# Optimization experiments

Hardware: AMD Instinct MI355X
Metric: run time of the kernel (lower is better)

## Reference

```python
import jax, jax.numpy as jnp
import numpy as np

NUM_HEADS = 16
D_MODEL = 1024
D_K = D_MODEL // NUM_HEADS


def setup_inputs() -> dict:
    key = jax.random.key(0)
    ks = jax.random.split(key, 11)
    B, S = 2, 2048
    s = 1.0 / np.sqrt(D_MODEL)
    return {
        "Q": jax.random.normal(ks[0], (B, S, D_MODEL), jnp.float32),
        "K": jax.random.normal(ks[1], (B, S, D_MODEL), jnp.float32),
        "V": jax.random.normal(ks[2], (B, S, D_MODEL), jnp.float32),
        "Wq": jax.random.normal(ks[3], (D_MODEL, D_MODEL), jnp.float32) * s,
        "bq": jnp.zeros((D_MODEL,), jnp.float32),
        "Wk": jax.random.normal(ks[4], (D_MODEL, D_MODEL), jnp.float32) * s,
        "bk": jnp.zeros((D_MODEL,), jnp.float32),
        "Wv": jax.random.normal(ks[5], (D_MODEL, D_MODEL), jnp.float32) * s,
        "bv": jnp.zeros((D_MODEL,), jnp.float32),
        "Wo": jax.random.normal(ks[6], (D_MODEL, D_MODEL), jnp.float32) * s,
        "bo": jnp.zeros((D_MODEL,), jnp.float32),
    }


def _split_heads(x):
    B, S, _ = x.shape
    return x.reshape(B, S, NUM_HEADS, D_K).transpose(0, 2, 1, 3)  # (B,H,S,Dk)


def reference(Q, K, V, Wq, bq, Wk, bk, Wv, bv, Wo, bo):
    q = _split_heads(Q @ Wq + bq)
    k = _split_heads(K @ Wk + bk)
    v = _split_heads(V @ Wv + bv)
    scores = jnp.einsum("bhqd,bhkd->bhqk", q, k) / jnp.sqrt(jnp.asarray(D_K, q.dtype))
    attn = jax.nn.softmax(scores, axis=-1)
    out = jnp.einsum("bhqk,bhkd->bhqd", attn, v)  # (B,H,S,Dk)
    B, H, S, Dk = out.shape
    combined = out.transpose(0, 2, 1, 3).reshape(B, S, H * Dk)
    return combined @ Wo + bo
```

## Files before the change

### kernel.cpp

```cpp
#include <hip/hip_runtime.h>
#include <stdint.h>

#define DM   1024
#define NH   16
#define DKH  64
#define SEQ  2048
#define NB   2

typedef __attribute__((ext_vector_type(8))) short  frag8;
typedef __attribute__((ext_vector_type(4))) short  frag4;
typedef __attribute__((ext_vector_type(4))) short  short4v;
typedef __attribute__((ext_vector_type(8))) short  short8v;
typedef __attribute__((ext_vector_type(4))) float  f32x4;

__device__ __forceinline__ unsigned short f2bf(float x){
  unsigned u = __float_as_uint(x);
  u += 0x7fffu + ((u >> 16) & 1u);
  return (unsigned short)(u >> 16);
}

__device__ __forceinline__ float dev_exp2(float x){
  return __builtin_amdgcn_exp2f(x);
}

#define GLOAD16(GP, LP) __builtin_amdgcn_global_load_lds( \
    (__attribute__((address_space(1))) void*)(GP), \
    (__attribute__((address_space(3))) void*)(LP), 16, 0, 0)

#define LDSFENCE() do{ asm volatile("" ::: "memory"); \
                       __builtin_amdgcn_sched_barrier(0); }while(0)



__global__ __launch_bounds__(256) void cast_qkv(const float* __restrict__ Q,
                                                const float* __restrict__ K,
                                                const float* __restrict__ V,
                                                short* __restrict__ dst){
  const int z = blockIdx.z;
  const float* src = (z == 0) ? Q : (z == 1 ? K : V);
  const int i = (blockIdx.x * 256 + threadIdx.x) * 4;
  float4 f = *(const float4*)(src + i);
  short4v s;
  s.x = (short)f2bf(f.x); s.y = (short)f2bf(f.y);
  s.z = (short)f2bf(f.z); s.w = (short)f2bf(f.w);
  *(short4v*)(dst + (long)z * (SEQ*NB*DM) + i) = s;
}

__global__ __launch_bounds__(256) void wtrans(const float* __restrict__ Wq,
                                              const float* __restrict__ Wk,
                                              const float* __restrict__ Wv,
                                              const float* __restrict__ Wo,
                                              short* __restrict__ wt){
  const int z = blockIdx.z;
  const float* W = (z == 0) ? Wq : (z == 1 ? Wk : (z == 2 ? Wv : Wo));
  short* out = wt + (long)z * (DM*DM);
  __shared__ float t[32][33];
  const int n0 = blockIdx.x * 32, k0 = blockIdx.y * 32;
  const int c = threadIdx.x & 31, r0 = threadIdx.x >> 5;
#pragma unroll
  for (int i = 0; i < 4; ++i){
    int r = r0 + i * 8;
    t[r][c] = W[(k0 + r) * DM + n0 + c];
  }
  __syncthreads();
#pragma unroll
  for (int i = 0; i < 4; ++i){
    int r = r0 + i * 8;
    out[(n0 + r) * DM + k0 + c] = (short)f2bf(t[c][r]);
  }
}

__device__ __forceinline__ void store_out(short* p, float v){ *p = (short)f2bf(v); }
__device__ __forceinline__ void store_out(float* p, float v){ *p = v; }

template<typename OT>
__global__ __launch_bounds__(512) void gemm_bt(const short* __restrict__ Abase, long Astride,
                                               const short* __restrict__ Btbase, long Btstride,
                                               const float* __restrict__ bias0,
                                               const float* __restrict__ bias1,
                                               const float* __restrict__ bias2,
                                               OT* __restrict__ Cbase, long Cstride,
                                               float qscale){
  const int z = blockIdx.z;
  const short* A  = Abase + (long)z * Astride;
  const short* Bt = Btbase + (long)z * Btstride;
  OT* C = Cbase + (long)z * Cstride;
  const float* bias = (z == 0) ? bias0 : (z == 1 ? bias1 : bias2);
  const float scale = (z == 0) ? qscale : 1.0f;
  const int KD = DM, ND = DM;

  __shared__ __align__(16) short As[2][128 * 64];
  __shared__ __align__(16) short Bs[2][128 * 64];

  const int tid = threadIdx.x;
  const int w = tid >> 6, lane = tid & 63, l15 = lane & 15, quad = lane >> 4;
  const int wy = w >> 1, wx = w & 1;
  const int bm = blockIdx.x * 128, bn = blockIdx.y * 128;
  const int lrow = lane >> 3;
  const int lcolsw = (((lane & 7) ^ lrow) & 7) * 8;

  f32x4 acc[2][4] = {};

#define GSTAGE(KT, BSEL) do{                                                    \
  _Pragma("unroll")                                                             \
  for (int i_ = 0; i_ < 2; ++i_){                                               \
    int j_ = w * 2 + i_;                                                        \
    GLOAD16(A  + (bm + j_ * 8 + lrow) * KD + (KT) * 64 + lcolsw,                \
            &As[BSEL][j_ * 512]);                                               \
    GLOAD16(Bt + (bn + j_ * 8 + lrow) * KD + (KT) * 64 + lcolsw,                \
            &Bs[BSEL][j_ * 512]);                                               \
  } }while(0)

#define GCOMPUTE(BS) do{                                                        \
  _Pragma("unroll") for (int ks = 0; ks < 2; ++ks){                             \
    frag8 af[2], bf_[4];                                                        \
    _Pragma("unroll") for (int mt = 0; mt < 2; ++mt)                            \
      af[mt] = *(const frag8*)&As[BS][(wy * 32 + mt * 16 + l15) * 64 +          \
                                      (((ks * 4 + quad) ^ (l15 & 7)) * 8)];     \
    _Pragma("unroll") for (int nt = 0; nt < 4; ++nt)                            \
      bf_[nt] = *(const frag8*)&Bs[BS][(wx * 64 + nt * 16 + l15) * 64 +         \
                                       (((ks * 4 + quad) ^ (l15 & 7)) * 8)];    \
    _Pragma("unroll") for (int mt = 0; mt < 2; ++mt)                            \
      _Pragma("unroll") for (int nt = 0; nt < 4; ++nt)                          \
        acc[mt][nt] = __builtin_amdgcn_mfma_f32_16x16x32_bf16(                  \
            af[mt], bf_[nt], acc[mt][nt], 0, 0, 0);                             \
  } }while(0)

  GSTAGE(0, 0);
  for (int t = 0; t < KD / 64 - 1; ++t){
    GSTAGE(t + 1, (t + 1) & 1);
    asm volatile("s_waitcnt vmcnt(4)" ::: "memory");
    __builtin_amdgcn_s_barrier();
    LDSFENCE();
    GCOMPUTE(t & 1);
    asm volatile("s_waitcnt lgkmcnt(0)" ::: "memory");
    __builtin_amdgcn_sched_barrier(0);
    __builtin_amdgcn_s_barrier();
  }
  asm volatile("s_waitcnt vmcnt(0)" ::: "memory");
  __builtin_amdgcn_s_barrier();
  LDSFENCE();
  GCOMPUTE(1);

#undef GSTAGE
#undef GCOMPUTE

#pragma unroll
  for (int mt = 0; mt < 2; ++mt){
#pragma unroll
    for (int r = 0; r < 4; ++r){
      int m = bm + wy * 32 + mt * 16 + quad * 4 + r;
#pragma unroll
      for (int nt = 0; nt < 4; ++nt){
        int n = bn + wx * 64 + nt * 16 + l15;
        float v = (acc[mt][nt][r] + bias[n]) * scale;
        store_out(&C[(long)m * ND + n], v);
      }
    }
  }
}

template<typename OT>
__global__ __launch_bounds__(512) void gemm64_bt(const short* __restrict__ A,
                                                 const short* __restrict__ Bt,
                                                 const float* __restrict__ bias,
                                                 OT* __restrict__ C,
                                                 float scale){
  const int KD = DM, ND = DM;
  __shared__ __align__(16) short As[2][64 * 64];
  __shared__ __align__(16) short Bs[2][128 * 64];
  const int tid = threadIdx.x;
  const int w = tid >> 6, lane = tid & 63, l15 = lane & 15, quad = lane >> 4;
  const int wy = w >> 1, wx = w & 1;
  const int bm = blockIdx.x * 64, bn = blockIdx.y * 128;
  const int lrow = lane >> 3;
  const int lcolsw = (((lane & 7) ^ lrow) & 7) * 8;
  f32x4 acc[4] = {};

#define GSTAGE64(KT, BSEL) do{                                                  \
  {                                                                             \
    int j_ = w;                                                                 \
    GLOAD16(A + (bm + j_ * 8 + lrow) * KD + (KT) * 64 + lcolsw,                 \
            &As[BSEL][j_ * 512]);                                               \
  }                                                                             \
  _Pragma("unroll")                                                             \
  for (int i_ = 0; i_ < 2; ++i_){                                               \
    int j_ = w * 2 + i_;                                                        \
    GLOAD16(Bt + (bn + j_ * 8 + lrow) * KD + (KT) * 64 + lcolsw,                \
            &Bs[BSEL][j_ * 512]);                                               \
  } }while(0)

#define GCOMPUTE64(BS) do{                                                      \
  _Pragma("unroll") for (int ks = 0; ks < 2; ++ks){                             \
    frag8 af, bf_[4];                                                           \
    af = *(const frag8*)&As[BS][(wy * 16 + l15) * 64 +                          \
                                (((ks * 4 + quad) ^ (l15 & 7)) * 8)];           \
    _Pragma("unroll") for (int nt = 0; nt < 4; ++nt)                            \
      bf_[nt] = *(const frag8*)&Bs[BS][(wx * 64 + nt * 16 + l15) * 64 +         \
                                       (((ks * 4 + quad) ^ (l15 & 7)) * 8)];    \
    _Pragma("unroll") for (int nt = 0; nt < 4; ++nt)                            \
      acc[nt] = __builtin_amdgcn_mfma_f32_16x16x32_bf16(                        \
          af, bf_[nt], acc[nt], 0, 0, 0);                                       \
  } }while(0)

  GSTAGE64(0, 0);
  for (int t = 0; t < KD / 64 - 1; ++t){
    GSTAGE64(t + 1, (t + 1) & 1);
    asm volatile("s_waitcnt vmcnt(3)" ::: "memory");
    __builtin_amdgcn_s_barrier();
    LDSFENCE();
    GCOMPUTE64(t & 1);
    asm volatile("s_waitcnt lgkmcnt(0)" ::: "memory");
    __builtin_amdgcn_sched_barrier(0);
    __builtin_amdgcn_s_barrier();
  }
  asm volatile("s_waitcnt vmcnt(0)" ::: "memory");
  __builtin_amdgcn_s_barrier();
  LDSFENCE();
  GCOMPUTE64(1);

#undef GSTAGE64
#undef GCOMPUTE64

#pragma unroll
  for (int r = 0; r < 4; ++r){
    int m = bm + wy * 16 + quad * 4 + r;
#pragma unroll
    for (int nt = 0; nt < 4; ++nt){
      int n = bn + wx * 64 + nt * 16 + l15;
      store_out(&C[(long)m * ND + n], (acc[nt][r] + bias[n]) * scale);
    }
  }
}

__global__ __launch_bounds__(256) void vtrans(const short* __restrict__ v,
                                              short* __restrict__ vt){
  const int bh = blockIdx.y;
  const int b = bh >> 4, h = bh & 15;
  const int s0 = blockIdx.x * 64;
  __shared__ short tT[64][66];
  const short* vb = v + ((long)(b * SEQ + s0)) * DM + h * DKH;
  for (int j = threadIdx.x; j < 512; j += 256){
    int row = j >> 3, off = (j & 7) * 8;
    short8v d = *(const short8v*)(vb + row * DM + off);
#pragma unroll
    for (int e = 0; e < 8; ++e) tT[off + e][row] = d[e];
  }
  __syncthreads();
  short* out = vt + (long)bh * (DKH * SEQ) + s0;
  for (int j = threadIdx.x; j < 512; j += 256){
    int dr = j >> 3, soff = (j & 7) * 8;
    short8v o;
#pragma unroll
    for (int e = 0; e < 8; ++e) o[e] = tT[dr][soff + e];
    *(short8v*)(out + dr * SEQ + soff) = o;
  }
}

__global__ __launch_bounds__(512) void flash(const short* __restrict__ q,
                                             const short* __restrict__ k,
                                             const short* __restrict__ vt,
                                             short* __restrict__ comb){
  const int bh = blockIdx.y;
  const int b = bh >> 4, h = bh & 15;
  const int q0 = blockIdx.x * 128;
  const int tid = threadIdx.x;
  const int w = tid >> 6, lane = tid & 63, l15 = lane & 15, quad = lane >> 4;

  __shared__ __align__(16) short Ks[3][64 * 64];
  __shared__ __align__(16) short Vs[3][64 * 64];

  frag8 aq[2];
  const short* qb = q + ((long)(b * SEQ + q0 + w * 16)) * DM + h * DKH;
#pragma unroll
  for (int ks = 0; ks < 2; ++ks)
    aq[ks] = *(const frag8*)(qb + l15 * DM + ks * 32 + quad * 8);

  frag8 ones8;
#pragma unroll
  for (int e = 0; e < 8; ++e) ones8[e] = (short)0x3F80;

  f32x4 O[4] = {};
  f32x4 Lacc = {0.f, 0.f, 0.f, 0.f};

  const short* kb  = k + ((long)b * SEQ) * DM + h * DKH;
  const short* vtb = vt + (long)bh * (DKH * SEQ);
  const int lrow8 = lane >> 3;
  const int lcolsw = (((lane & 7) ^ lrow8) & 7) * 8;

#define STAGE(KT, BSEL) do{                                                     \
  int jj_ = w;                                                                  \
  int kr_ = 32 * (jj_ >> 2) + 8 * ((jj_ * 2 + (lrow8 >> 2)) & 3)                \
          + 4 * ((jj_ >> 1) & 1) + (lrow8 & 3);                                 \
  GLOAD16(kb  + ((KT) * 64 + kr_) * DM + lcolsw,        &Ks[BSEL][jj_ * 512]);  \
  GLOAD16(vtb + (jj_ * 8 + lrow8) * SEQ + (KT) * 64 + lcolsw,                   \
          &Vs[BSEL][jj_ * 512]);                                                \
}while(0)

#define COMPUTE(BS) do{                                                         \
  __builtin_amdgcn_s_setprio(1);                                                \
  f32x4 scT[4];                                                                 \
  _Pragma("unroll") for (int nt = 0; nt < 4; ++nt)                              \
    scT[nt] = (f32x4){0.f, 0.f, 0.f, 0.f};                                      \
  _Pragma("unroll") for (int ks = 0; ks < 2; ++ks){                             \
    _Pragma("unroll") for (int nt = 0; nt < 4; ++nt){                           \
      frag8 ak = *(const frag8*)&Ks[BS][(nt * 16 + l15) * 64 +                  \
                                        (((ks * 4 + quad) ^ (l15 & 7)) * 8)];   \
      scT[nt] = __builtin_amdgcn_mfma_f32_16x16x32_bf16(                        \
          ak, aq[ks], scT[nt], 0, 0, 0);                                        \
    }                                                                           \
  }                                                                             \
  frag8 ap8[2];                                                                 \
  _Pragma("unroll") for (int c2 = 0; c2 < 2; ++c2){                             \
    union { frag8 f8; unsigned u[4]; } P_;                                      \
    _Pragma("unroll") for (int hf = 0; hf < 2; ++hf){                           \
      unsigned u0 = __float_as_uint(dev_exp2(scT[2*c2+hf][0])) + 0x8000u;       \
      unsigned u1 = __float_as_uint(dev_exp2(scT[2*c2+hf][1])) + 0x8000u;       \
      unsigned u2 = __float_as_uint(dev_exp2(scT[2*c2+hf][2])) + 0x8000u;       \
      unsigned u3 = __float_as_uint(dev_exp2(scT[2*c2+hf][3])) + 0x8000u;       \
      P_.u[hf * 2]     = (u0 >> 16) | (u1 & 0xffff0000u);                       \
      P_.u[hf * 2 + 1] = (u2 >> 16) | (u3 & 0xffff0000u);                       \
    }                                                                           \
    ap8[c2] = P_.f8;                                                            \
  }                                                                             \
  _Pragma("unroll") for (int c2 = 0; c2 < 2; ++c2){                             \
    _Pragma("unroll") for (int dt = 0; dt < 4; ++dt){                           \
      frag8 bv8 = *(const frag8*)&Vs[BS][(dt * 16 + l15) * 64 +                 \
                                         (((c2 * 4 + quad) ^ (l15 & 7)) * 8)];  \
      O[dt] = __builtin_amdgcn_mfma_f32_16x16x32_bf16(                          \
          ap8[c2], bv8, O[dt], 0, 0, 0);                                        \
    }                                                                           \
    Lacc = __builtin_amdgcn_mfma_f32_16x16x32_bf16(                             \
        ap8[c2], ones8, Lacc, 0, 0, 0);                                         \
  }                                                                             \
  __builtin_amdgcn_s_setprio(0);                                                \
}while(0)

#define ITER(KT, BC, BSNEXT) do{                                                \
  STAGE((KT) + 2, BSNEXT);                                                      \
  asm volatile("s_waitcnt vmcnt(4)" ::: "memory");                              \
  __builtin_amdgcn_s_barrier();                                                 \
  LDSFENCE();                                                                   \
  COMPUTE(BC);                                                                  \
  asm volatile("s_waitcnt lgkmcnt(0)" ::: "memory");                            \
  __builtin_amdgcn_sched_barrier(0);                                            \
  __builtin_amdgcn_s_barrier();                                                 \
}while(0)

  STAGE(0, 0);
  STAGE(1, 1);
  for (int kt = 0; kt < SEQ / 64 - 2; kt += 3){
    ITER(kt,     0, 2);
    ITER(kt + 1, 1, 0);
    ITER(kt + 2, 2, 1);
  }
  asm volatile("s_waitcnt vmcnt(2)" ::: "memory");
  __builtin_amdgcn_s_barrier();
  LDSFENCE();
  COMPUTE(0);
  asm volatile("s_waitcnt vmcnt(0)" ::: "memory");
  __builtin_amdgcn_s_barrier();
  LDSFENCE();
  COMPUTE(1);

#undef ITER
#undef COMPUTE
#undef STAGE

  short* ob = comb + ((long)(b * SEQ + q0 + w * 16)) * DM + h * DKH;
#pragma unroll
  for (int r = 0; r < 4; ++r){
    float inv = 1.f / Lacc[r];
#pragma unroll
    for (int dt = 0; dt < 4; ++dt)
      ob[(quad * 4 + r) * DM + dt * 16 + l15] = (short)f2bf(O[dt][r] * inv);
  }
}

extern "C" void kernel_launch(void* const* d_in, const int* in_sizes, int n_in,
                              void* d_out, int out_size, void* d_ws, size_t ws_size,
                              hipStream_t stream){
  const float* Q  = (const float*)d_in[0];
  const float* K  = (const float*)d_in[1];
  const float* V  = (const float*)d_in[2];
  const float* Wq = (const float*)d_in[3];
  const float* bq = (const float*)d_in[4];
  const float* Wk = (const float*)d_in[5];
  const float* bk = (const float*)d_in[6];
  const float* Wv = (const float*)d_in[7];
  const float* bv = (const float*)d_in[8];
  const float* Wo = (const float*)d_in[9];
  const float* bo = (const float*)d_in[10];
  float* out = (float*)d_out;

  const long TEN = (long)NB * SEQ * DM;
  const long WEL = (long)DM * DM;
  short* ws   = (short*)d_ws;
  short* xc   = ws;
  short* wt   = xc + 3 * TEN;
  short* qkv  = wt + 4 * WEL;
  short* vtr  = qkv + 3 * TEN;
  short* comb = vtr + TEN;

  cast_qkv<<<dim3(4096, 1, 3), 256, 0, stream>>>(Q, K, V, xc);
  wtrans<<<dim3(32, 32, 4), 256, 0, stream>>>(Wq, Wk, Wv, Wo, wt);
  gemm_bt<short><<<dim3(32, 8, 3), 512, 0, stream>>>(xc, TEN, wt, WEL, bq, bk, bv,
                                                     qkv, TEN, 0.125f * 1.44269504f);
  vtrans<<<dim3(32, 32), 256, 0, stream>>>(qkv + 2 * TEN, vtr);
  flash<<<dim3(16, 32), 512, 0, stream>>>(qkv, qkv + TEN, vtr, comb);
  gemm64_bt<float><<<dim3(64, 8), 512, 0, stream>>>(comb, wt + 3 * WEL, bo, out, 1.0f);
  (void)in_sizes; (void)n_in; (void)out_size; (void)ws_size;
}
```

Baseline: 213.9 us.

## Fuse V transpose into QKV GEMM epilogue and drop separate vtrans kernel

The QKV projection GEMM now writes the V slice directly in transposed per-head layout, staging the tile through reused LDS before writing 16-byte chunks. This removes the standalone vtrans kernel launch and its round trip of V through global memory. The flash kernel's bf16 packing of exp values is also rewritten as a simpler per-element round-and-shift. In exchange, the GEMM epilogue for the V slice gains extra barriers and an LDS transpose.

```diff
diff --git a/kernel.cpp b/kernel.cpp
--- a/kernel.cpp
+++ b/kernel.cpp
@@ -80,6 +80,7 @@
                                                const float* __restrict__ bias1,
                                                const float* __restrict__ bias2,
                                                OT* __restrict__ Cbase, long Cstride,
+                                               short* __restrict__ vtr,
                                                float qscale){
   const int z = blockIdx.z;
   const short* A  = Abase + (long)z * Astride;
@@ -89,8 +90,9 @@
   const float scale = (z == 0) ? qscale : 1.0f;
   const int KD = DM, ND = DM;
 
-  __shared__ __align__(16) short As[2][128 * 64];
-  __shared__ __align__(16) short Bs[2][128 * 64];
+  __shared__ __align__(16) short SMEM[4 * 128 * 64];
+#define AS_(BSEL, IDX) SMEM[(BSEL) * 8192 + (IDX)]
+#define BSS(BSEL, IDX) SMEM[16384 + (BSEL) * 8192 + (IDX)]
 
   const int tid = threadIdx.x;
   const int w = tid >> 6, lane = tid & 63, l15 = lane & 15, quad = lane >> 4;
@@ -106,20 +108,20 @@
   for (int i_ = 0; i_ < 2; ++i_){                                               \
     int j_ = w * 2 + i_;                                                        \
     GLOAD16(A  + (bm + j_ * 8 + lrow) * KD + (KT) * 64 + lcolsw,                \
-            &As[BSEL][j_ * 512]);                                               \
+            &AS_(BSEL, j_ * 512));                                              \
     GLOAD16(Bt + (bn + j_ * 8 + lrow) * KD + (KT) * 64 + lcolsw,                \
-            &Bs[BSEL][j_ * 512]);                                               \
+            &BSS(BSEL, j_ * 512));                                              \
   } }while(0)
 
 #define GCOMPUTE(BS) do{                                                        \
   _Pragma("unroll") for (int ks = 0; ks < 2; ++ks){                             \
     frag8 af[2], bf_[4];                                                        \
     _Pragma("unroll") for (int mt = 0; mt < 2; ++mt)                            \
-      af[mt] = *(const frag8*)&As[BS][(wy * 32 + mt * 16 + l15) * 64 +          \
-                                      (((ks * 4 + quad) ^ (l15 & 7)) * 8)];     \
+      af[mt] = *(const frag8*)&AS_(BS, (wy * 32 + mt * 16 + l15) * 64 +         \
+                                       (((ks * 4 + quad) ^ (l15 & 7)) * 8));    \
     _Pragma("unroll") for (int nt = 0; nt < 4; ++nt)                            \
-      bf_[nt] = *(const frag8*)&Bs[BS][(wx * 64 + nt * 16 + l15) * 64 +         \
-                                       (((ks * 4 + quad) ^ (l15 & 7)) * 8)];    \
+      bf_[nt] = *(const frag8*)&BSS(BS, (wx * 64 + nt * 16 + l15) * 64 +        \
+                                        (((ks * 4 + quad) ^ (l15 & 7)) * 8));   \
     _Pragma("unroll") for (int mt = 0; mt < 2; ++mt)                            \
       _Pragma("unroll") for (int nt = 0; nt < 4; ++nt)                          \
         acc[mt][nt] = __builtin_amdgcn_mfma_f32_16x16x32_bf16(                  \
@@ -145,19 +147,54 @@
 #undef GSTAGE
 #undef GCOMPUTE
 
-#pragma unroll
-  for (int mt = 0; mt < 2; ++mt){
-#pragma unroll
-    for (int r = 0; r < 4; ++r){
-      int m = bm + wy * 32 + mt * 16 + quad * 4 + r;
-#pragma unroll
-      for (int nt = 0; nt < 4; ++nt){
-        int n = bn + wx * 64 + nt * 16 + l15;
-        float v = (acc[mt][nt][r] + bias[n]) * scale;
-        store_out(&C[(long)m * ND + n], v);
+  if (vtr == nullptr || z != 2){
+#pragma unroll
+    for (int mt = 0; mt < 2; ++mt){
+#pragma unroll
+      for (int r = 0; r < 4; ++r){
+        int m = bm + wy * 32 + mt * 16 + quad * 4 + r;
+#pragma unroll
+        for (int nt = 0; nt < 4; ++nt){
+          int n = bn + wx * 64 + nt * 16 + l15;
+          float v = (acc[mt][nt][r] + bias[n]) * scale;
+          store_out(&C[(long)m * ND + n], v);
+        }
       }
     }
-  }
+  } else {
+    const int PIT = 136;
+    short* T = SMEM;
+    asm volatile("s_waitcnt lgkmcnt(0)" ::: "memory");
+    __builtin_amdgcn_s_barrier();
+    LDSFENCE();
+#pragma unroll
+    for (int mt = 0; mt < 2; ++mt){
+#pragma unroll
+      for (int nt = 0; nt < 4; ++nt){
+        int n = wx * 64 + nt * 16 + l15;
+        int m0 = wy * 32 + mt * 16 + quad * 4;
+        short4v v4;
+#pragma unroll
+        for (int r = 0; r < 4; ++r)
+          v4[r] = (short)f2bf(acc[mt][nt][r] + bias[bn + n]);
+        *(short4v*)&T[n * PIT + m0] = v4;
+      }
+    }
+    asm volatile("s_waitcnt lgkmcnt(0)" ::: "memory");
+    __builtin_amdgcn_s_barrier();
+    LDSFENCE();
+    const int b_ = bm >> 11, s0 = bm & (SEQ - 1);
+#pragma unroll
+    for (int it = 0; it < 4; ++it){
+      int c = it * 512 + tid;
+      int nl = c >> 4, ms = (c & 15) * 8;
+      short8v v8 = *(const short8v*)&T[nl * PIT + ms];
+      int h_ = (bn >> 6) + (nl >> 6), dk = nl & 63;
+      *(short8v*)(vtr + ((long)(b_ * 16 + h_) * 64 + dk) * SEQ + s0 + ms) = v8;
+    }
+  }
+#undef AS_
+#undef BSS
 }
 
 template<typename OT>
@@ -233,30 +270,6 @@
   }
 }
 
-__global__ __launch_bounds__(256) void vtrans(const short* __restrict__ v,
-                                              short* __restrict__ vt){
-  const int bh = blockIdx.y;
-  const int b = bh >> 4, h = bh & 15;
-  const int s0 = blockIdx.x * 64;
-  __shared__ short tT[64][66];
-  const short* vb = v + ((long)(b * SEQ + s0)) * DM + h * DKH;
-  for (int j = threadIdx.x; j < 512; j += 256){
-    int row = j >> 3, off = (j & 7) * 8;
-    short8v d = *(const short8v*)(vb + row * DM + off);
-#pragma unroll
-    for (int e = 0; e < 8; ++e) tT[off + e][row] = d[e];
-  }
-  __syncthreads();
-  short* out = vt + (long)bh * (DKH * SEQ) + s0;
-  for (int j = threadIdx.x; j < 512; j += 256){
-    int dr = j >> 3, soff = (j & 7) * 8;
-    short8v o;
-#pragma unroll
-    for (int e = 0; e < 8; ++e) o[e] = tT[dr][soff + e];
-    *(short8v*)(out + dr * SEQ + soff) = o;
-  }
-}
-
 __global__ __launch_bounds__(512) void flash(const short* __restrict__ q,
                                              const short* __restrict__ k,
                                              const short* __restrict__ vt,
@@ -312,16 +325,13 @@
   }                                                                             \
   frag8 ap8[2];                                                                 \
   _Pragma("unroll") for (int c2 = 0; c2 < 2; ++c2){                             \
-    union { frag8 f8; unsigned u[4]; } P_;                                      \
-    _Pragma("unroll") for (int hf = 0; hf < 2; ++hf){                           \
-      unsigned u0 = __float_as_uint(dev_exp2(scT[2*c2+hf][0])) + 0x8000u;       \
-      unsigned u1 = __float_as_uint(dev_exp2(scT[2*c2+hf][1])) + 0x8000u;       \
-      unsigned u2 = __float_as_uint(dev_exp2(scT[2*c2+hf][2])) + 0x8000u;       \
-      unsigned u3 = __float_as_uint(dev_exp2(scT[2*c2+hf][3])) + 0x8000u;       \
-      P_.u[hf * 2]     = (u0 >> 16) | (u1 & 0xffff0000u);                       \
-      P_.u[hf * 2 + 1] = (u2 >> 16) | (u3 & 0xffff0000u);                       \
-    }                                                                           \
-    ap8[c2] = P_.f8;                                                            \
+    frag8 p8;                                                                   \
+    _Pragma("unroll") for (int hf = 0; hf < 2; ++hf)                            \
+      _Pragma("unroll") for (int r = 0; r < 4; ++r){                            \
+        float e = dev_exp2(scT[2 * c2 + hf][r]);                                \
+        p8[hf * 4 + r] = (short)((__float_as_uint(e) + 0x8000u) >> 16);         \
+      }                                                                         \
+    ap8[c2] = p8;                                                               \
   }                                                                             \
   _Pragma("unroll") for (int c2 = 0; c2 < 2; ++c2){                             \
     _Pragma("unroll") for (int dt = 0; dt < 4; ++dt){                           \
@@ -405,8 +415,7 @@
   cast_qkv<<<dim3(4096, 1, 3), 256, 0, stream>>>(Q, K, V, xc);
   wtrans<<<dim3(32, 32, 4), 256, 0, stream>>>(Wq, Wk, Wv, Wo, wt);
   gemm_bt<short><<<dim3(32, 8, 3), 512, 0, stream>>>(xc, TEN, wt, WEL, bq, bk, bv,
-                                                     qkv, TEN, 0.125f * 1.44269504f);
-  vtrans<<<dim3(32, 32), 256, 0, stream>>>(qkv + 2 * TEN, vtr);
+                                                     qkv, TEN, vtr, 0.125f * 1.44269504f);
   flash<<<dim3(16, 32), 512, 0, stream>>>(qkv, qkv + TEN, vtr, comb);
   gemm64_bt<float><<<dim3(64, 8), 512, 0, stream>>>(comb, wt + 3 * WEL, bo, out, 1.0f);
   (void)in_sizes; (void)n_in; (void)out_size; (void)ws_size;
```

Result: faster. 206.4 us (-3.5%).
